# Kernel optimization log

Measured on AMD Instinct MI355X. Metric: run time of the kernel, lower is better.

The kernel has to match this reference:

```python
import jax, jax.numpy as jnp
import numpy as np

THR = 0.2          # config['thr']
BORDER_RM = 2      # config['border_rm']
TEMP = 0.1         # config['dsmax_temperature']


def setup_inputs() -> dict:
    key = jax.random.key(0)
    k0, k1 = jax.random.split(key)
    N, C = 2, 256
    h0c, w0c, h1c, w1c = 60, 80, 60, 80
    return {
        "feat_c0": jax.random.normal(k0, (N, h0c * w0c, C), dtype=jnp.float32),
        "feat_c1": jax.random.normal(k1, (N, h1c * w1c, C), dtype=jnp.float32),
        "h0c": h0c, "w0c": w0c, "h1c": h1c, "w1c": w1c,
    }


def _valid_1d(n: int, b: int):
    # True in the interior [b, n-b), False on the border — matches mask_border writes
    return jnp.zeros((n,), dtype=bool).at[b:n - b].set(True)


def reference(feat_c0, feat_c1, h0c, w0c, h1c, w1c):
    N, L, C = feat_c0.shape
    S = feat_c1.shape[1]
    scale = 1.0 / (C ** 0.5)
    f0 = feat_c0 * scale
    f1 = feat_c1 * scale

    # similarity + dual softmax  -> conf_matrix [N, L, S]
    sim = jnp.einsum('nlc,nsc->nls', f0, f1) / TEMP
    conf = jax.nn.softmax(sim, axis=1) * jax.nn.softmax(sim, axis=2)

    # threshold + border removal (mask_border, vectorized as an interior mask)
    mask = conf > THR
    b = BORDER_RM
    border = (_valid_1d(h0c, b)[:, None, None, None]
              & _valid_1d(w0c, b)[None, :, None, None]
              & _valid_1d(h1c, b)[None, None, :, None]
              & _valid_1d(w1c, b)[None, None, None, :])  # [h0c,w0c,h1c,w1c]
    mask = (mask.reshape(N, h0c, w0c, h1c, w1c) & border[None]).reshape(N, L, S)

    # mutual nearest neighbor
    mask = mask \
        & (conf == conf.max(axis=2, keepdims=True)) \
        & (conf == conf.max(axis=1, keepdims=True))

    # match extraction, expressed densely (static shapes for jit):
    # mask_v[b,i] = row i of pair b has a match; j_ids its column; mconf its confidence
    mask_v = mask.any(axis=2)                               # [N, L]
    j_ids = jnp.argmax(mask, axis=2)                        # [N, L] (first True)
    mconf = jnp.take_along_axis(conf, j_ids[:, :, None], axis=2)[..., 0]
    mconf = jnp.where(mask_v, mconf, 0.0)                   # [N, L]

    # coarse keypoint coords for matched columns: (x, y) = (j % w1c, j // w1c)
    mkpts1_c = jnp.stack([j_ids % w1c, j_ids // w1c], axis=-1)  # [N, L, 2]

    return conf, mask_v, j_ids, mkpts1_c, mconf
```

## Files before the change

### kernel.cpp

```cpp
#include <hip/hip_runtime.h>

typedef _Float16 half8 __attribute__((ext_vector_type(8)));
typedef float f32x4 __attribute__((ext_vector_type(4)));

#define NB 2
#define LS 4800
#define CCH 256
#define W0 80
#define W1 80
#define THRV 0.2f
#define SQS 0.19764235376052370f

#define TN 38
#define PADL 4864
#define NWG (TN * TN * NB)
#define CPX (NWG / 8)

#define OF_RST  0
#define OF_CST  19200
#define OF_RWM  38400
#define OF_CAND 48000
#define OF_CLM  57600
#define OF_PROW 67200
#define OF_PCOL (67200 + 739328)
#define OF_AH   (67200 + 2*739328)
#define OF_BH   (OF_AH + 1228800)

#define O_MASKV 46080000ull
#define O_JIDS  46089600ull
#define O_MKPT  46099200ull
#define O_MCONF 46118400ull

__device__ __forceinline__ void load_lds16(const void* g, void* l) {
    __builtin_amdgcn_global_load_lds((const __attribute__((address_space(1))) void*)g,
                                     (__attribute__((address_space(3))) void*)l, 16, 0, 0);
}

__device__ __forceinline__ void swizzle_ids(int& n, int& by, int& bx) {
    const int orig = ((int)blockIdx.z * TN + (int)blockIdx.y) * TN + (int)blockIdx.x;
    const int wg = (orig & 7) * CPX + (orig >> 3);
    n = wg / (TN * TN);
    const int rem = wg % (TN * TN);
    by = rem / TN; bx = rem % TN;
}

__global__ __launch_bounds__(256) void conv_half(const float* __restrict__ A,
                                                 const float* __restrict__ B,
                                                 float* __restrict__ ws) {
    const int which = blockIdx.y;
    const float* src = which ? B : A;
    _Float16* dst = (_Float16*)(ws + (which ? OF_BH : OF_AH));
    const int idx = blockIdx.x * 256 + threadIdx.x;
    const float4 v = ((const float4*)src)[idx];
    union { _Float16 h[4]; uint2 u; } p;
    p.h[0] = (_Float16)(v.x * SQS);
    p.h[1] = (_Float16)(v.y * SQS);
    p.h[2] = (_Float16)(v.z * SQS);
    p.h[3] = (_Float16)(v.w * SQS);
    ((uint2*)dst)[idx] = p.u;
}

__device__ __forceinline__ void gemm_core(const _Float16* __restrict__ Ah,
                                          const _Float16* __restrict__ Bh,
                                          _Float16* smA, _Float16* smB,
                                          const int bx, const int by,
                                          const int tid, f32x4 (&acc)[4][4]) {
    const int lane = tid & 63, w = tid >> 6;
    const int wx = w & 1, wy = w >> 1;
    const int m = lane & 15, quad = lane >> 4;
    const int rr = lane >> 2;
    const int q = (lane & 3) ^ ((lane >> 3) & 3);

    const _Float16* ga[2];
    const _Float16* gb[2];
#pragma unroll
    for (int i = 0; i < 2; i++) {
        const int c = w * 2 + i;
        int gra = by * 128 + c * 16 + rr; gra = gra < LS ? gra : LS - 1;
        int grb = bx * 128 + c * 16 + rr; grb = grb < LS ? grb : LS - 1;
        ga[i] = Ah + (size_t)gra * CCH + q * 8;
        gb[i] = Bh + (size_t)grb * CCH + q * 8;
    }

#pragma unroll
    for (int i = 0; i < 2; i++) {
        const int c = w * 2 + i;
        load_lds16(ga[i], &smA[c * 512]);
        load_lds16(gb[i], &smB[c * 512]);
    }

    for (int kt = 0; kt < 8; kt++) {
        __syncthreads();
        const int cur = (kt & 1) * 4096;
        if (kt < 7) {
            const int nxt = 4096 - cur;
            const int ko = (kt + 1) * 32;
#pragma unroll
            for (int i = 0; i < 2; i++) {
                const int c = w * 2 + i;
                load_lds16(ga[i] + ko, &smA[nxt + c * 512]);
                load_lds16(gb[i] + ko, &smB[nxt + c * 512]);
            }
        }
        half8 Af[4], Bf[4];
#pragma unroll
        for (int a = 0; a < 4; a++) {
            const int rl = wy * 64 + a * 16 + m;
            const int sl = rl * 4 + (quad ^ ((rl >> 1) & 3));
            Af[a] = *(const half8*)&smA[cur + sl * 8];
        }
#pragma unroll
        for (int b = 0; b < 4; b++) {
            const int cl = wx * 64 + b * 16 + m;
            const int sl = cl * 4 + (quad ^ ((cl >> 1) & 3));
            Bf[b] = *(const half8*)&smB[cur + sl * 8];
        }
#pragma unroll
        for (int a = 0; a < 4; a++)
#pragma unroll
            for (int b = 0; b < 4; b++)
                acc[a][b] = __builtin_amdgcn_mfma_f32_16x16x32_f16(Af[a], Bf[b], acc[a][b], 0, 0, 0);
    }
    __syncthreads();
}

__global__ __launch_bounds__(256, 3) void gemm_stats(float* __restrict__ ws) {
    __shared__ __align__(16) union {
        struct { _Float16 A[8192]; _Float16 B[8192]; } st;
        struct { float rs[128][2][2]; float cs[128][2][2]; } red;
    } sm;
    int n, by, bx;
    swizzle_ids(n, by, bx);
    const _Float16* Ah = (const _Float16*)(ws + OF_AH) + (size_t)n * LS * CCH;
    const _Float16* Bh = (const _Float16*)(ws + OF_BH) + (size_t)n * LS * CCH;
    const int tid = threadIdx.x;
    const int lane = tid & 63, w = tid >> 6;
    const int wx = w & 1, wy = w >> 1;
    const int m = lane & 15, quad = lane >> 4;

    f32x4 acc[4][4];
    {
        f32x4 z = {0.f, 0.f, 0.f, 0.f};
#pragma unroll
        for (int a = 0; a < 4; a++)
#pragma unroll
            for (int b = 0; b < 4; b++) acc[a][b] = z;
    }
    gemm_core(Ah, Bh, sm.st.A, sm.st.B, bx, by, tid, acc);

    const int l0 = by * 128, s0 = bx * 128;
    bool bval[4];
#pragma unroll
    for (int b = 0; b < 4; b++) bval[b] = (s0 + wx * 64 + b * 16 + m) < LS;

    float T = -1e30f;
#pragma unroll
    for (int a = 0; a < 4; a++)
#pragma unroll
        for (int reg = 0; reg < 4; reg++) {
            if ((l0 + wy * 64 + a * 16 + quad * 4 + reg) < LS) {
#pragma unroll
                for (int b = 0; b < 4; b++)
                    if (bval[b]) T = fmaxf(T, acc[a][b][reg]);
            }
        }
#pragma unroll
    for (int d = 1; d < 64; d <<= 1) T = fmaxf(T, __shfl_xor(T, d, 64));

#pragma unroll
    for (int a = 0; a < 4; a++)
#pragma unroll
        for (int reg = 0; reg < 4; reg++) {
            const bool rv = (l0 + wy * 64 + a * 16 + quad * 4 + reg) < LS;
#pragma unroll
            for (int b = 0; b < 4; b++)
                acc[a][b][reg] = (rv && bval[b]) ? __expf(acc[a][b][reg] - T) : 0.f;
        }

#pragma unroll
    for (int a = 0; a < 4; a++)
#pragma unroll
        for (int reg = 0; reg < 4; reg++) {
            float s = acc[a][0][reg] + acc[a][1][reg] + acc[a][2][reg] + acc[a][3][reg];
#pragma unroll
            for (int d = 1; d < 16; d <<= 1) s += __shfl_xor(s, d, 64);
            if (m == 0) {
                const int rl = wy * 64 + a * 16 + quad * 4 + reg;
                sm.red.rs[rl][wx][0] = T; sm.red.rs[rl][wx][1] = s;
            }
        }
#pragma unroll
    for (int b = 0; b < 4; b++) {
        float s = 0.f;
#pragma unroll
        for (int a = 0; a < 4; a++)
#pragma unroll
            for (int reg = 0; reg < 4; reg++) s += acc[a][b][reg];
        s += __shfl_xor(s, 16, 64);
        s += __shfl_xor(s, 32, 64);
        if (quad == 0) {
            const int cl = wx * 64 + b * 16 + m;
            sm.red.cs[cl][wy][0] = T; sm.red.cs[cl][wy][1] = s;
        }
    }
    __syncthreads();
    if (tid < 128) {
        const float m0 = sm.red.rs[tid][0][0], v0 = sm.red.rs[tid][0][1];
        const float m1 = sm.red.rs[tid][1][0], v1 = sm.red.rs[tid][1][1];
        const float nm = fmaxf(m0, m1);
        const float s = v0 * __expf(m0 - nm) + v1 * __expf(m1 - nm);
        ((float2*)(ws + OF_PROW))[((size_t)n * PADL + by * 128 + tid) * TN + bx] = make_float2(nm, s);
    } else {
        const int t = tid - 128;
        const float m0 = sm.red.cs[t][0][0], v0 = sm.red.cs[t][0][1];
        const float m1 = sm.red.cs[t][1][0], v1 = sm.red.cs[t][1][1];
        const float nm = fmaxf(m0, m1);
        const float s = v0 * __expf(m0 - nm) + v1 * __expf(m1 - nm);
        ((float2*)(ws + OF_PCOL))[((size_t)n * PADL + bx * 128 + t) * TN + by] = make_float2(nm, s);
    }
}

__global__ __launch_bounds__(256) void combine_stats(float* __restrict__ ws) {
    const int idx = blockIdx.x * 256 + threadIdx.x;
    const int half_ = idx >= 9600;
    const int i = idx - half_ * 9600;
    const int n = i / LS, r = i % LS;
    const float2* P = (const float2*)(ws + (half_ ? OF_PCOL : OF_PROW)) + ((size_t)n * PADL + r) * TN;
    float M = -1e30f, S = 0.f;
    for (int b = 0; b < TN; b++) {
        const float2 p = P[b];
        const float nm = fmaxf(M, p.x);
        S = S * __expf(M - nm) + p.y * __expf(p.x - nm);
        M = nm;
    }
    ((float2*)(ws + (half_ ? OF_CST : OF_RST)))[n * LS + r] = make_float2(M, 1.0f / S);
}

__global__ __launch_bounds__(256, 3) void gemm_conf(float* __restrict__ out,
                                                    float* __restrict__ ws) {
    __shared__ __align__(16) union {
        struct { _Float16 A[8192]; _Float16 B[8192]; } st;
        struct { float rst[128][2]; float cst[128][2];
                 float rsv[128][2][2]; float csv[128][2]; } ep;
    } sm;
    int n, by, bx;
    swizzle_ids(n, by, bx);
    const _Float16* Ah = (const _Float16*)(ws + OF_AH) + (size_t)n * LS * CCH;
    const _Float16* Bh = (const _Float16*)(ws + OF_BH) + (size_t)n * LS * CCH;
    const int tid = threadIdx.x;
    const int lane = tid & 63, w = tid >> 6;
    const int wx = w & 1, wy = w >> 1;
    const int m = lane & 15, quad = lane >> 4;

    f32x4 acc[4][4];
    {
        f32x4 z = {0.f, 0.f, 0.f, 0.f};
#pragma unroll
        for (int a = 0; a < 4; a++)
#pragma unroll
            for (int b = 0; b < 4; b++) acc[a][b] = z;
    }
    gemm_core(Ah, Bh, sm.st.A, sm.st.B, bx, by, tid, acc);

    const int l0 = by * 128, s0 = bx * 128;
    if (tid < 128) {
        int r = l0 + tid; r = r < LS ? r : LS - 1;
        const float2 v = ((const float2*)(ws + OF_RST))[n * LS + r];
        sm.ep.rst[tid][0] = v.x; sm.ep.rst[tid][1] = v.y;
    } else {
        const int t = tid - 128;
        int c = s0 + t; c = c < LS ? c : LS - 1;
        const float2 v = ((const float2*)(ws + OF_CST))[n * LS + c];
        sm.ep.cst[t][0] = v.x; sm.ep.cst[t][1] = v.y;
    }
    __syncthreads();

    float* On = out + (size_t)n * LS * LS;
    float colm[4] = {-1.f, -1.f, -1.f, -1.f};
    bool bval[4]; int gc4[4]; float cmx[4], csi[4];
#pragma unroll
    for (int b = 0; b < 4; b++) {
        const int cl = wx * 64 + b * 16 + m;
        gc4[b] = s0 + cl;
        bval[b] = gc4[b] < LS;
        cmx[b] = sm.ep.cst[cl][0]; csi[b] = sm.ep.cst[cl][1];
    }
#pragma unroll
    for (int a = 0; a < 4; a++) {
#pragma unroll
        for (int reg = 0; reg < 4; reg++) {
            const int rl = wy * 64 + a * 16 + quad * 4 + reg;
            const int gr = l0 + rl;
            const float rm = sm.ep.rst[rl][0], rsi = sm.ep.rst[rl][1];
            const bool rv = gr < LS;
            float bestv = -1.f; int besti = 0;
#pragma unroll
            for (int b = 0; b < 4; b++) {
                const float c = __expf(2.f * acc[a][b][reg] - rm - cmx[b]) * (rsi * csi[b]);
                if (rv && bval[b]) {
                    On[(size_t)gr * LS + gc4[b]] = c;
                    if (c > bestv) { bestv = c; besti = gc4[b]; }
                    colm[b] = fmaxf(colm[b], c);
                }
            }
#pragma unroll
            for (int d = 1; d < 16; d <<= 1) {
                const float ov = __shfl_xor(bestv, d, 64);
                const int oi = __shfl_xor(besti, d, 64);
                if (ov > bestv || (ov == bestv && oi < besti)) { bestv = ov; besti = oi; }
            }
            if (m == 0) {
                sm.ep.rsv[rl][wx][0] = bestv;
                sm.ep.rsv[rl][wx][1] = __int_as_float(besti);
            }
        }
    }
#pragma unroll
    for (int b = 0; b < 4; b++) {
        float v = colm[b];
        v = fmaxf(v, __shfl_xor(v, 16, 64));
        v = fmaxf(v, __shfl_xor(v, 32, 64));
        if (quad == 0) sm.ep.csv[wx * 64 + b * 16 + m][wy] = v;
    }
    __syncthreads();
    if (tid < 128) {
        const float v0 = sm.ep.rsv[tid][0][0]; const int i0 = __float_as_int(sm.ep.rsv[tid][0][1]);
        const float v1 = sm.ep.rsv[tid][1][0]; const int i1 = __float_as_int(sm.ep.rsv[tid][1][1]);
        float bv; int bi;
        if (v0 > v1 || (v0 == v1 && i0 <= i1)) { bv = v0; bi = i0; } else { bv = v1; bi = i1; }
        ((float2*)(ws + OF_PROW))[((size_t)n * PADL + by * 128 + tid) * TN + bx] =
            make_float2(bv, __int_as_float(bi));
    } else {
        const int t = tid - 128;
        const float v = fmaxf(sm.ep.csv[t][0], sm.ep.csv[t][1]);
        (ws + OF_PCOL)[((size_t)n * PADL + bx * 128 + t) * TN + by] = v;
    }
}

__global__ __launch_bounds__(256) void combine_max(float* __restrict__ ws) {
    const int idx = blockIdx.x * 256 + threadIdx.x;
    const int half_ = idx >= 9600;
    const int i = idx - half_ * 9600;
    const int n = i / LS, r = i % LS;
    if (!half_) {
        const float2* P = (const float2*)(ws + OF_PROW) + ((size_t)n * PADL + r) * TN;
        float bv = -2.f; int bi = 0;
        for (int b = 0; b < TN; b++) {
            const float2 p = P[b];
            const int pi = __float_as_int(p.y);
            if (p.x > bv || (p.x == bv && pi < bi)) { bv = p.x; bi = pi; }
        }
        ws[OF_RWM + i] = bv;
        ((int*)ws)[OF_CAND + i] = bi;
    } else {
        const float* P = ws + OF_PCOL + ((size_t)n * PADL + r) * TN;
        float v = -2.f;
        for (int b = 0; b < TN; b++) v = fmaxf(v, P[b]);
        ws[OF_CLM + i] = v;
    }
}

__global__ __launch_bounds__(256) void match_pass(const float* __restrict__ ws,
                                                  float* __restrict__ out) {
    const int idx = blockIdx.x * 256 + threadIdx.x;
    if (idx >= NB * LS) return;
    const int n = idx / LS, l = idx % LS;
    const float rwm = ws[OF_RWM + idx];
    const int cand = ((const int*)ws)[OF_CAND + idx];
    const float clm = ws[OF_CLM + n * LS + cand];
    const int y0 = l / W0, x0 = l % W0;
    const int y1 = cand / W1, x1 = cand % W1;
    const bool b0 = (y0 >= 2 && y0 < 58 && x0 >= 2 && x0 < 78);
    const bool b1 = (y1 >= 2 && y1 < 58 && x1 >= 2 && x1 < 78);
    const bool matched = (rwm > THRV) && b0 && b1 && (rwm == clm);
    const int j = matched ? cand : 0;
    out[O_MASKV + idx] = matched ? 1.f : 0.f;
    out[O_JIDS + idx] = (float)j;
    out[O_MKPT + (size_t)idx * 2 + 0] = (float)(j % W1);
    out[O_MKPT + (size_t)idx * 2 + 1] = (float)(j / W1);
    out[O_MCONF + idx] = matched ? rwm : 0.f;
}

extern "C" void kernel_launch(void* const* d_in, const int* in_sizes, int n_in,
                              void* d_out, int out_size, void* d_ws, size_t ws_size,
                              hipStream_t stream) {
    const float* f0 = (const float*)d_in[0];
    const float* f1 = (const float*)d_in[1];
    float* out = (float*)d_out;
    float* ws = (float*)d_ws;

    conv_half<<<dim3(2400, 2), 256, 0, stream>>>(f0, f1, ws);
    gemm_stats<<<dim3(TN, TN, NB), 256, 0, stream>>>(ws);
    combine_stats<<<75, 256, 0, stream>>>(ws);
    gemm_conf<<<dim3(TN, TN, NB), 256, 0, stream>>>(out, ws);
    combine_max<<<75, 256, 0, stream>>>(ws);
    match_pass<<<38, 256, 0, stream>>>(ws, out);
}
```

Measured before the change: 306.4 us.

## Use 256x128 GEMM tiles with 512-thread blocks and nontemporal conf stores

Doubles the row extent of each workgroup tile to 256 rows using 8 waves, so each B tile loaded into LDS is reused across twice as many rows. This halves the workgroup count and the number of column-statistics partials, and the partial reductions and the XCD swizzle are rewritten to match. The conf matrix output is now written with nontemporal stores to reduce cache pollution. Larger blocks and more LDS per block may lower occupancy, and the uneven XCD split adds some risk.

```diff
diff --git a/kernel.cpp b/kernel.cpp
--- a/kernel.cpp
+++ b/kernel.cpp
@@ -11,10 +11,10 @@
 #define THRV 0.2f
 #define SQS 0.19764235376052370f
 
-#define TN 38
+#define TN  38
+#define TNM 19
 #define PADL 4864
-#define NWG (TN * TN * NB)
-#define CPX (NWG / 8)
+#define NWG (TN * TNM * NB)
 
 #define OF_RST  0
 #define OF_CST  19200
@@ -37,10 +37,11 @@
 }
 
 __device__ __forceinline__ void swizzle_ids(int& n, int& by, int& bx) {
-    const int orig = ((int)blockIdx.z * TN + (int)blockIdx.y) * TN + (int)blockIdx.x;
-    const int wg = (orig & 7) * CPX + (orig >> 3);
-    n = wg / (TN * TN);
-    const int rem = wg % (TN * TN);
+    const int orig = ((int)blockIdx.z * TNM + (int)blockIdx.y) * TN + (int)blockIdx.x;
+    const int xcd = orig & 7, t = orig >> 3;
+    const int wg = (xcd < 4 ? xcd * 181 : 724 + (xcd - 4) * 180) + t;
+    n = wg / (TN * TNM);
+    const int rem = wg % (TN * TNM);
     by = rem / TN; bx = rem % TN;
 }
 
@@ -72,48 +73,44 @@
     const int q = (lane & 3) ^ ((lane >> 3) & 3);
 
     const _Float16* ga[2];
-    const _Float16* gb[2];
-#pragma unroll
-    for (int i = 0; i < 2; i++) {
-        const int c = w * 2 + i;
-        int gra = by * 128 + c * 16 + rr; gra = gra < LS ? gra : LS - 1;
-        int grb = bx * 128 + c * 16 + rr; grb = grb < LS ? grb : LS - 1;
-        ga[i] = Ah + (size_t)gra * CCH + q * 8;
-        gb[i] = Bh + (size_t)grb * CCH + q * 8;
-    }
-
-#pragma unroll
-    for (int i = 0; i < 2; i++) {
-        const int c = w * 2 + i;
-        load_lds16(ga[i], &smA[c * 512]);
-        load_lds16(gb[i], &smB[c * 512]);
-    }
+    const _Float16* gb0;
+    {
+#pragma unroll
+        for (int i = 0; i < 2; i++) {
+            const int c = w * 2 + i;
+            int gra = by * 256 + c * 16 + rr; gra = gra < LS ? gra : LS - 1;
+            ga[i] = Ah + (size_t)gra * CCH + q * 8;
+        }
+        int grb = bx * 128 + w * 16 + rr; grb = grb < LS ? grb : LS - 1;
+        gb0 = Bh + (size_t)grb * CCH + q * 8;
+    }
+
+#pragma unroll
+    for (int i = 0; i < 2; i++) load_lds16(ga[i], &smA[(w * 2 + i) * 512]);
+    load_lds16(gb0, &smB[w * 512]);
 
     for (int kt = 0; kt < 8; kt++) {
         __syncthreads();
-        const int cur = (kt & 1) * 4096;
+        const int curA = (kt & 1) * 8192, curB = (kt & 1) * 4096;
         if (kt < 7) {
-            const int nxt = 4096 - cur;
             const int ko = (kt + 1) * 32;
 #pragma unroll
-            for (int i = 0; i < 2; i++) {
-                const int c = w * 2 + i;
-                load_lds16(ga[i] + ko, &smA[nxt + c * 512]);
-                load_lds16(gb[i] + ko, &smB[nxt + c * 512]);
-            }
+            for (int i = 0; i < 2; i++)
+                load_lds16(ga[i] + ko, &smA[(8192 - curA) + (w * 2 + i) * 512]);
+            load_lds16(gb0 + ko, &smB[(4096 - curB) + w * 512]);
         }
         half8 Af[4], Bf[4];
 #pragma unroll
         for (int a = 0; a < 4; a++) {
             const int rl = wy * 64 + a * 16 + m;
             const int sl = rl * 4 + (quad ^ ((rl >> 1) & 3));
-            Af[a] = *(const half8*)&smA[cur + sl * 8];
+            Af[a] = *(const half8*)&smA[curA + sl * 8];
         }
 #pragma unroll
         for (int b = 0; b < 4; b++) {
             const int cl = wx * 64 + b * 16 + m;
             const int sl = cl * 4 + (quad ^ ((cl >> 1) & 3));
-            Bf[b] = *(const half8*)&smB[cur + sl * 8];
+            Bf[b] = *(const half8*)&smB[curB + sl * 8];
         }
 #pragma unroll
         for (int a = 0; a < 4; a++)
@@ -124,10 +121,10 @@
     __syncthreads();
 }
 
-__global__ __launch_bounds__(256, 3) void gemm_stats(float* __restrict__ ws) {
+__global__ __launch_bounds__(512, 4) void gemm_stats(float* __restrict__ ws) {
     __shared__ __align__(16) union {
-        struct { _Float16 A[8192]; _Float16 B[8192]; } st;
-        struct { float rs[128][2][2]; float cs[128][2][2]; } red;
+        struct { _Float16 A[2][8192]; _Float16 B[2][4096]; } st;
+        struct { float rs[256][2][2]; float cs[128][4][2]; } red;
     } sm;
     int n, by, bx;
     swizzle_ids(n, by, bx);
@@ -146,9 +143,9 @@
 #pragma unroll
             for (int b = 0; b < 4; b++) acc[a][b] = z;
     }
-    gemm_core(Ah, Bh, sm.st.A, sm.st.B, bx, by, tid, acc);
-
-    const int l0 = by * 128, s0 = bx * 128;
+    gemm_core(Ah, Bh, &sm.st.A[0][0], &sm.st.B[0][0], bx, by, tid, acc);
+
+    const int l0 = by * 256, s0 = bx * 128;
     bool bval[4];
 #pragma unroll
     for (int b = 0; b < 4; b++) bval[b] = (s0 + wx * 64 + b * 16 + m) < LS;
@@ -204,19 +201,23 @@
         }
     }
     __syncthreads();
-    if (tid < 128) {
+    if (tid < 256) {
         const float m0 = sm.red.rs[tid][0][0], v0 = sm.red.rs[tid][0][1];
         const float m1 = sm.red.rs[tid][1][0], v1 = sm.red.rs[tid][1][1];
         const float nm = fmaxf(m0, m1);
         const float s = v0 * __expf(m0 - nm) + v1 * __expf(m1 - nm);
-        ((float2*)(ws + OF_PROW))[((size_t)n * PADL + by * 128 + tid) * TN + bx] = make_float2(nm, s);
-    } else {
-        const int t = tid - 128;
-        const float m0 = sm.red.cs[t][0][0], v0 = sm.red.cs[t][0][1];
-        const float m1 = sm.red.cs[t][1][0], v1 = sm.red.cs[t][1][1];
-        const float nm = fmaxf(m0, m1);
-        const float s = v0 * __expf(m0 - nm) + v1 * __expf(m1 - nm);
-        ((float2*)(ws + OF_PCOL))[((size_t)n * PADL + bx * 128 + t) * TN + by] = make_float2(nm, s);
+        ((float2*)(ws + OF_PROW))[((size_t)n * PADL + l0 + tid) * TN + bx] = make_float2(nm, s);
+    } else if (tid < 384) {
+        const int t = tid - 256;
+        float M = sm.red.cs[t][0][0], S = sm.red.cs[t][0][1];
+#pragma unroll
+        for (int k = 1; k < 4; k++) {
+            const float mo = sm.red.cs[t][k][0], so = sm.red.cs[t][k][1];
+            const float nm = fmaxf(M, mo);
+            S = S * __expf(M - nm) + so * __expf(mo - nm);
+            M = nm;
+        }
+        ((float2*)(ws + OF_PCOL))[((size_t)n * PADL + s0 + t) * TNM + by] = make_float2(M, S);
     }
 }
 
@@ -225,23 +226,34 @@
     const int half_ = idx >= 9600;
     const int i = idx - half_ * 9600;
     const int n = i / LS, r = i % LS;
-    const float2* P = (const float2*)(ws + (half_ ? OF_PCOL : OF_PROW)) + ((size_t)n * PADL + r) * TN;
     float M = -1e30f, S = 0.f;
-    for (int b = 0; b < TN; b++) {
-        const float2 p = P[b];
-        const float nm = fmaxf(M, p.x);
-        S = S * __expf(M - nm) + p.y * __expf(p.x - nm);
-        M = nm;
-    }
-    ((float2*)(ws + (half_ ? OF_CST : OF_RST)))[n * LS + r] = make_float2(M, 1.0f / S);
-}
-
-__global__ __launch_bounds__(256, 3) void gemm_conf(float* __restrict__ out,
+    if (!half_) {
+        const float2* P = (const float2*)(ws + OF_PROW) + ((size_t)n * PADL + r) * TN;
+        for (int b = 0; b < TN; b++) {
+            const float2 p = P[b];
+            const float nm = fmaxf(M, p.x);
+            S = S * __expf(M - nm) + p.y * __expf(p.x - nm);
+            M = nm;
+        }
+        ((float2*)(ws + OF_RST))[n * LS + r] = make_float2(M, 1.0f / S);
+    } else {
+        const float2* P = (const float2*)(ws + OF_PCOL) + ((size_t)n * PADL + r) * TNM;
+        for (int b = 0; b < TNM; b++) {
+            const float2 p = P[b];
+            const float nm = fmaxf(M, p.x);
+            S = S * __expf(M - nm) + p.y * __expf(p.x - nm);
+            M = nm;
+        }
+        ((float2*)(ws + OF_CST))[n * LS + r] = make_float2(M, 1.0f / S);
+    }
+}
+
+__global__ __launch_bounds__(512, 4) void gemm_conf(float* __restrict__ out,
                                                     float* __restrict__ ws) {
     __shared__ __align__(16) union {
-        struct { _Float16 A[8192]; _Float16 B[8192]; } st;
-        struct { float rst[128][2]; float cst[128][2];
-                 float rsv[128][2][2]; float csv[128][2]; } ep;
+        struct { _Float16 A[2][8192]; _Float16 B[2][4096]; } st;
+        struct { float rst[256][2]; float cst[128][2];
+                 float rsv[256][2][2]; float csv[128][4]; } ep;
     } sm;
     int n, by, bx;
     swizzle_ids(n, by, bx);
@@ -260,15 +272,15 @@
 #pragma unroll
             for (int b = 0; b < 4; b++) acc[a][b] = z;
     }
-    gemm_core(Ah, Bh, sm.st.A, sm.st.B, bx, by, tid, acc);
-
-    const int l0 = by * 128, s0 = bx * 128;
-    if (tid < 128) {
+    gemm_core(Ah, Bh, &sm.st.A[0][0], &sm.st.B[0][0], bx, by, tid, acc);
+
+    const int l0 = by * 256, s0 = bx * 128;
+    if (tid < 256) {
         int r = l0 + tid; r = r < LS ? r : LS - 1;
         const float2 v = ((const float2*)(ws + OF_RST))[n * LS + r];
         sm.ep.rst[tid][0] = v.x; sm.ep.rst[tid][1] = v.y;
-    } else {
-        const int t = tid - 128;
+    } else if (tid < 384) {
+        const int t = tid - 256;
         int c = s0 + t; c = c < LS ? c : LS - 1;
         const float2 v = ((const float2*)(ws + OF_CST))[n * LS + c];
         sm.ep.cst[t][0] = v.x; sm.ep.cst[t][1] = v.y;
@@ -298,7 +310,7 @@
             for (int b = 0; b < 4; b++) {
                 const float c = __expf(2.f * acc[a][b][reg] - rm - cmx[b]) * (rsi * csi[b]);
                 if (rv && bval[b]) {
-                    On[(size_t)gr * LS + gc4[b]] = c;
+                    __builtin_nontemporal_store(c, &On[(size_t)gr * LS + gc4[b]]);
                     if (c > bestv) { bestv = c; besti = gc4[b]; }
                     colm[b] = fmaxf(colm[b], c);
                 }
@@ -323,17 +335,18 @@
         if (quad == 0) sm.ep.csv[wx * 64 + b * 16 + m][wy] = v;
     }
     __syncthreads();
-    if (tid < 128) {
+    if (tid < 256) {
         const float v0 = sm.ep.rsv[tid][0][0]; const int i0 = __float_as_int(sm.ep.rsv[tid][0][1]);
         const float v1 = sm.ep.rsv[tid][1][0]; const int i1 = __float_as_int(sm.ep.rsv[tid][1][1]);
         float bv; int bi;
         if (v0 > v1 || (v0 == v1 && i0 <= i1)) { bv = v0; bi = i0; } else { bv = v1; bi = i1; }
-        ((float2*)(ws + OF_PROW))[((size_t)n * PADL + by * 128 + tid) * TN + bx] =
+        ((float2*)(ws + OF_PROW))[((size_t)n * PADL + l0 + tid) * TN + bx] =
             make_float2(bv, __int_as_float(bi));
-    } else {
-        const int t = tid - 128;
-        const float v = fmaxf(sm.ep.csv[t][0], sm.ep.csv[t][1]);
-        (ws + OF_PCOL)[((size_t)n * PADL + bx * 128 + t) * TN + by] = v;
+    } else if (tid < 384) {
+        const int t = tid - 256;
+        const float v = fmaxf(fmaxf(sm.ep.csv[t][0], sm.ep.csv[t][1]),
+                              fmaxf(sm.ep.csv[t][2], sm.ep.csv[t][3]));
+        (ws + OF_PCOL)[((size_t)n * PADL + s0 + t) * TNM + by] = v;
     }
 }
 
@@ -353,9 +366,9 @@
         ws[OF_RWM + i] = bv;
         ((int*)ws)[OF_CAND + i] = bi;
     } else {
-        const float* P = ws + OF_PCOL + ((size_t)n * PADL + r) * TN;
+        const float* P = ws + OF_PCOL + ((size_t)n * PADL + r) * TNM;
         float v = -2.f;
-        for (int b = 0; b < TN; b++) v = fmaxf(v, P[b]);
+        for (int b = 0; b < TNM; b++) v = fmaxf(v, P[b]);
         ws[OF_CLM + i] = v;
     }
 }
@@ -390,9 +403,9 @@
     float* ws = (float*)d_ws;
 
     conv_half<<<dim3(2400, 2), 256, 0, stream>>>(f0, f1, ws);
-    gemm_stats<<<dim3(TN, TN, NB), 256, 0, stream>>>(ws);
+    gemm_stats<<<dim3(TN, TNM, NB), 512, 0, stream>>>(ws);
     combine_stats<<<75, 256, 0, stream>>>(ws);
-    gemm_conf<<<dim3(TN, TN, NB), 256, 0, stream>>>(out, ws);
+    gemm_conf<<<dim3(TN, TNM, NB), 512, 0, stream>>>(out, ws);
     combine_max<<<75, 256, 0, stream>>>(ws);
     match_pass<<<38, 256, 0, stream>>>(ws, out);
 }
```

New measurement: 310.6 us. About the same (+1.4%).

## Use 8 waves per GEMM tile and add mask-free fast path for interior tiles

Applied to the files above, without the earlier changes.

Both GEMM kernels go from 256 to 512 threads per 128x128 tile. Each wave now covers 32x64 instead of 64x64, so accumulator registers per thread halve and more waves can hide latency. The cross-wave column reductions are widened from 2 to 4 partials to match. Interior tiles skip the per-element bounds checks in the softmax-statistics and confidence epilogues. The cost is less MFMA work per wave between barriers, with more synchronisation and LDS traffic relative to compute.

```diff
diff --git a/kernel.cpp b/kernel.cpp
--- a/kernel.cpp
+++ b/kernel.cpp
@@ -64,48 +64,34 @@
                                           const _Float16* __restrict__ Bh,
                                           _Float16* smA, _Float16* smB,
                                           const int bx, const int by,
-                                          const int tid, f32x4 (&acc)[4][4]) {
+                                          const int tid, f32x4 (&acc)[2][4]) {
     const int lane = tid & 63, w = tid >> 6;
     const int wx = w & 1, wy = w >> 1;
     const int m = lane & 15, quad = lane >> 4;
     const int rr = lane >> 2;
     const int q = (lane & 3) ^ ((lane >> 3) & 3);
 
-    const _Float16* ga[2];
-    const _Float16* gb[2];
-#pragma unroll
-    for (int i = 0; i < 2; i++) {
-        const int c = w * 2 + i;
-        int gra = by * 128 + c * 16 + rr; gra = gra < LS ? gra : LS - 1;
-        int grb = bx * 128 + c * 16 + rr; grb = grb < LS ? grb : LS - 1;
-        ga[i] = Ah + (size_t)gra * CCH + q * 8;
-        gb[i] = Bh + (size_t)grb * CCH + q * 8;
-    }
-
-#pragma unroll
-    for (int i = 0; i < 2; i++) {
-        const int c = w * 2 + i;
-        load_lds16(ga[i], &smA[c * 512]);
-        load_lds16(gb[i], &smB[c * 512]);
-    }
+    int gra = by * 128 + w * 16 + rr; gra = gra < LS ? gra : LS - 1;
+    int grb = bx * 128 + w * 16 + rr; grb = grb < LS ? grb : LS - 1;
+    const _Float16* ga = Ah + (size_t)gra * CCH + q * 8;
+    const _Float16* gb = Bh + (size_t)grb * CCH + q * 8;
+
+    load_lds16(ga, &smA[w * 512]);
+    load_lds16(gb, &smB[w * 512]);
 
     for (int kt = 0; kt < 8; kt++) {
         __syncthreads();
         const int cur = (kt & 1) * 4096;
         if (kt < 7) {
+            const int ko = (kt + 1) * 32;
             const int nxt = 4096 - cur;
-            const int ko = (kt + 1) * 32;
-#pragma unroll
-            for (int i = 0; i < 2; i++) {
-                const int c = w * 2 + i;
-                load_lds16(ga[i] + ko, &smA[nxt + c * 512]);
-                load_lds16(gb[i] + ko, &smB[nxt + c * 512]);
-            }
-        }
-        half8 Af[4], Bf[4];
-#pragma unroll
-        for (int a = 0; a < 4; a++) {
-            const int rl = wy * 64 + a * 16 + m;
+            load_lds16(ga + ko, &smA[nxt + w * 512]);
+            load_lds16(gb + ko, &smB[nxt + w * 512]);
+        }
+        half8 Af[2], Bf[4];
+#pragma unroll
+        for (int a = 0; a < 2; a++) {
+            const int rl = wy * 32 + a * 16 + m;
             const int sl = rl * 4 + (quad ^ ((rl >> 1) & 3));
             Af[a] = *(const half8*)&smA[cur + sl * 8];
         }
@@ -116,7 +102,7 @@
             Bf[b] = *(const half8*)&smB[cur + sl * 8];
         }
 #pragma unroll
-        for (int a = 0; a < 4; a++)
+        for (int a = 0; a < 2; a++)
 #pragma unroll
             for (int b = 0; b < 4; b++)
                 acc[a][b] = __builtin_amdgcn_mfma_f32_16x16x32_f16(Af[a], Bf[b], acc[a][b], 0, 0, 0);
@@ -124,10 +110,10 @@
     __syncthreads();
 }
 
-__global__ __launch_bounds__(256, 3) void gemm_stats(float* __restrict__ ws) {
+__global__ __launch_bounds__(512, 6) void gemm_stats(float* __restrict__ ws) {
     __shared__ __align__(16) union {
-        struct { _Float16 A[8192]; _Float16 B[8192]; } st;
-        struct { float rs[128][2][2]; float cs[128][2][2]; } red;
+        struct { _Float16 A[2][4096]; _Float16 B[2][4096]; } st;
+        struct { float rs[128][2][2]; float cs[128][4][2]; } red;
     } sm;
     int n, by, bx;
     swizzle_ids(n, by, bx);
@@ -138,54 +124,77 @@
     const int wx = w & 1, wy = w >> 1;
     const int m = lane & 15, quad = lane >> 4;
 
-    f32x4 acc[4][4];
+    f32x4 acc[2][4];
     {
         f32x4 z = {0.f, 0.f, 0.f, 0.f};
 #pragma unroll
-        for (int a = 0; a < 4; a++)
+        for (int a = 0; a < 2; a++)
 #pragma unroll
             for (int b = 0; b < 4; b++) acc[a][b] = z;
     }
-    gemm_core(Ah, Bh, sm.st.A, sm.st.B, bx, by, tid, acc);
+    gemm_core(Ah, Bh, &sm.st.A[0][0], &sm.st.B[0][0], bx, by, tid, acc);
 
     const int l0 = by * 128, s0 = bx * 128;
-    bool bval[4];
-#pragma unroll
-    for (int b = 0; b < 4; b++) bval[b] = (s0 + wx * 64 + b * 16 + m) < LS;
+    const bool full = (by < 37) & (bx < 37);
 
     float T = -1e30f;
-#pragma unroll
-    for (int a = 0; a < 4; a++)
-#pragma unroll
-        for (int reg = 0; reg < 4; reg++) {
-            if ((l0 + wy * 64 + a * 16 + quad * 4 + reg) < LS) {
+    if (full) {
+#pragma unroll
+        for (int a = 0; a < 2; a++)
+#pragma unroll
+            for (int reg = 0; reg < 4; reg++)
+#pragma unroll
+                for (int b = 0; b < 4; b++) T = fmaxf(T, acc[a][b][reg]);
+    } else {
+        bool bval[4];
+#pragma unroll
+        for (int b = 0; b < 4; b++) bval[b] = (s0 + wx * 64 + b * 16 + m) < LS;
+#pragma unroll
+        for (int a = 0; a < 2; a++)
+#pragma unroll
+            for (int reg = 0; reg < 4; reg++) {
+                if ((l0 + wy * 32 + a * 16 + quad * 4 + reg) < LS) {
+#pragma unroll
+                    for (int b = 0; b < 4; b++)
+                        if (bval[b]) T = fmaxf(T, acc[a][b][reg]);
+                }
+            }
+    }
+#pragma unroll
+    for (int d = 1; d < 64; d <<= 1) T = fmaxf(T, __shfl_xor(T, d, 64));
+
+    if (full) {
+#pragma unroll
+        for (int a = 0; a < 2; a++)
+#pragma unroll
+            for (int reg = 0; reg < 4; reg++)
 #pragma unroll
                 for (int b = 0; b < 4; b++)
-                    if (bval[b]) T = fmaxf(T, acc[a][b][reg]);
+                    acc[a][b][reg] = __expf(acc[a][b][reg] - T);
+    } else {
+        bool bval[4];
+#pragma unroll
+        for (int b = 0; b < 4; b++) bval[b] = (s0 + wx * 64 + b * 16 + m) < LS;
+#pragma unroll
+        for (int a = 0; a < 2; a++)
+#pragma unroll
+            for (int reg = 0; reg < 4; reg++) {
+                const bool rv = (l0 + wy * 32 + a * 16 + quad * 4 + reg) < LS;
+#pragma unroll
+                for (int b = 0; b < 4; b++)
+                    acc[a][b][reg] = (rv && bval[b]) ? __expf(acc[a][b][reg] - T) : 0.f;
             }
-        }
-#pragma unroll
-    for (int d = 1; d < 64; d <<= 1) T = fmaxf(T, __shfl_xor(T, d, 64));
-
-#pragma unroll
-    for (int a = 0; a < 4; a++)
-#pragma unroll
-        for (int reg = 0; reg < 4; reg++) {
-            const bool rv = (l0 + wy * 64 + a * 16 + quad * 4 + reg) < LS;
-#pragma unroll
-            for (int b = 0; b < 4; b++)
-                acc[a][b][reg] = (rv && bval[b]) ? __expf(acc[a][b][reg] - T) : 0.f;
-        }
-
-#pragma unroll
-    for (int a = 0; a < 4; a++)
+    }
+
+#pragma unroll
+    for (int a = 0; a < 2; a++)
 #pragma unroll
         for (int reg = 0; reg < 4; reg++) {
             float s = acc[a][0][reg] + acc[a][1][reg] + acc[a][2][reg] + acc[a][3][reg];
 #pragma unroll
             for (int d = 1; d < 16; d <<= 1) s += __shfl_xor(s, d, 64);
             if (m == 0) {
-                const int rl = wy * 64 + a * 16 + quad * 4 + reg;
+                const int rl = wy * 32 + a * 16 + quad * 4 + reg;
                 sm.red.rs[rl][wx][0] = T; sm.red.rs[rl][wx][1] = s;
             }
         }
@@ -193,7 +202,7 @@
     for (int b = 0; b < 4; b++) {
         float s = 0.f;
 #pragma unroll
-        for (int a = 0; a < 4; a++)
+        for (int a = 0; a < 2; a++)
 #pragma unroll
             for (int reg = 0; reg < 4; reg++) s += acc[a][b][reg];
         s += __shfl_xor(s, 16, 64);
@@ -209,14 +218,18 @@
         const float m1 = sm.red.rs[tid][1][0], v1 = sm.red.rs[tid][1][1];
         const float nm = fmaxf(m0, m1);
         const float s = v0 * __expf(m0 - nm) + v1 * __expf(m1 - nm);
-        ((float2*)(ws + OF_PROW))[((size_t)n * PADL + by * 128 + tid) * TN + bx] = make_float2(nm, s);
-    } else {
+        ((float2*)(ws + OF_PROW))[((size_t)n * PADL + l0 + tid) * TN + bx] = make_float2(nm, s);
+    } else if (tid < 256) {
         const int t = tid - 128;
-        const float m0 = sm.red.cs[t][0][0], v0 = sm.red.cs[t][0][1];
-        const float m1 = sm.red.cs[t][1][0], v1 = sm.red.cs[t][1][1];
-        const float nm = fmaxf(m0, m1);
-        const float s = v0 * __expf(m0 - nm) + v1 * __expf(m1 - nm);
-        ((float2*)(ws + OF_PCOL))[((size_t)n * PADL + bx * 128 + t) * TN + by] = make_float2(nm, s);
+        float M = sm.red.cs[t][0][0], S = sm.red.cs[t][0][1];
+#pragma unroll
+        for (int k = 1; k < 4; k++) {
+            const float mo = sm.red.cs[t][k][0], so = sm.red.cs[t][k][1];
+            const float nm = fmaxf(M, mo);
+            S = S * __expf(M - nm) + so * __expf(mo - nm);
+            M = nm;
+        }
+        ((float2*)(ws + OF_PCOL))[((size_t)n * PADL + s0 + t) * TN + by] = make_float2(M, S);
     }
 }
 
@@ -236,12 +249,12 @@
     ((float2*)(ws + (half_ ? OF_CST : OF_RST)))[n * LS + r] = make_float2(M, 1.0f / S);
 }
 
-__global__ __launch_bounds__(256, 3) void gemm_conf(float* __restrict__ out,
+__global__ __launch_bounds__(512, 6) void gemm_conf(float* __restrict__ out,
                                                     float* __restrict__ ws) {
     __shared__ __align__(16) union {
-        struct { _Float16 A[8192]; _Float16 B[8192]; } st;
+        struct { _Float16 A[2][4096]; _Float16 B[2][4096]; } st;
         struct { float rst[128][2]; float cst[128][2];
-                 float rsv[128][2][2]; float csv[128][2]; } ep;
+                 float rsv[128][2][2]; float csv[128][4]; } ep;
     } sm;
     int n, by, bx;
     swizzle_ids(n, by, bx);
@@ -252,22 +265,23 @@
     const int wx = w & 1, wy = w >> 1;
     const int m = lane & 15, quad = lane >> 4;
 
-    f32x4 acc[4][4];
+    f32x4 acc[2][4];
     {
         f32x4 z = {0.f, 0.f, 0.f, 0.f};
 #pragma unroll
-        for (int a = 0; a < 4; a++)
+        for (int a = 0; a < 2; a++)
 #pragma unroll
             for (int b = 0; b < 4; b++) acc[a][b] = z;
     }
-    gemm_core(Ah, Bh, sm.st.A, sm.st.B, bx, by, tid, acc);
+    gemm_core(Ah, Bh, &sm.st.A[0][0], &sm.st.B[0][0], bx, by, tid, acc);
 
     const int l0 = by * 128, s0 = bx * 128;
+    const bool full = (by < 37) & (bx < 37);
     if (tid < 128) {
         int r = l0 + tid; r = r < LS ? r : LS - 1;
         const float2 v = ((const float2*)(ws + OF_RST))[n * LS + r];
         sm.ep.rst[tid][0] = v.x; sm.ep.rst[tid][1] = v.y;
-    } else {
+    } else if (tid < 256) {
         const int t = tid - 128;
         int c = s0 + t; c = c < LS ? c : LS - 1;
         const float2 v = ((const float2*)(ws + OF_CST))[n * LS + c];
@@ -277,41 +291,73 @@
 
     float* On = out + (size_t)n * LS * LS;
     float colm[4] = {-1.f, -1.f, -1.f, -1.f};
-    bool bval[4]; int gc4[4]; float cmx[4], csi[4];
+    int gc4[4]; float cmx[4], csi[4];
 #pragma unroll
     for (int b = 0; b < 4; b++) {
         const int cl = wx * 64 + b * 16 + m;
         gc4[b] = s0 + cl;
-        bval[b] = gc4[b] < LS;
         cmx[b] = sm.ep.cst[cl][0]; csi[b] = sm.ep.cst[cl][1];
     }
-#pragma unroll
-    for (int a = 0; a < 4; a++) {
-#pragma unroll
-        for (int reg = 0; reg < 4; reg++) {
-            const int rl = wy * 64 + a * 16 + quad * 4 + reg;
-            const int gr = l0 + rl;
-            const float rm = sm.ep.rst[rl][0], rsi = sm.ep.rst[rl][1];
-            const bool rv = gr < LS;
-            float bestv = -1.f; int besti = 0;
-#pragma unroll
-            for (int b = 0; b < 4; b++) {
-                const float c = __expf(2.f * acc[a][b][reg] - rm - cmx[b]) * (rsi * csi[b]);
-                if (rv && bval[b]) {
+    if (full) {
+#pragma unroll
+        for (int a = 0; a < 2; a++) {
+#pragma unroll
+            for (int reg = 0; reg < 4; reg++) {
+                const int rl = wy * 32 + a * 16 + quad * 4 + reg;
+                const int gr = l0 + rl;
+                const float rm = sm.ep.rst[rl][0], rsi = sm.ep.rst[rl][1];
+                float bestv = -1.f; int besti = 0;
+#pragma unroll
+                for (int b = 0; b < 4; b++) {
+                    const float c = __expf(2.f * acc[a][b][reg] - rm - cmx[b]) * (rsi * csi[b]);
                     On[(size_t)gr * LS + gc4[b]] = c;
                     if (c > bestv) { bestv = c; besti = gc4[b]; }
                     colm[b] = fmaxf(colm[b], c);
                 }
+#pragma unroll
+                for (int d = 1; d < 16; d <<= 1) {
+                    const float ov = __shfl_xor(bestv, d, 64);
+                    const int oi = __shfl_xor(besti, d, 64);
+                    if (ov > bestv || (ov == bestv && oi < besti)) { bestv = ov; besti = oi; }
+                }
+                if (m == 0) {
+                    sm.ep.rsv[rl][wx][0] = bestv;
+                    sm.ep.rsv[rl][wx][1] = __int_as_float(besti);
+                }
             }
-#pragma unroll
-            for (int d = 1; d < 16; d <<= 1) {
-                const float ov = __shfl_xor(bestv, d, 64);
-                const int oi = __shfl_xor(besti, d, 64);
-                if (ov > bestv || (ov == bestv && oi < besti)) { bestv = ov; besti = oi; }
-            }
-            if (m == 0) {
-                sm.ep.rsv[rl][wx][0] = bestv;
-                sm.ep.rsv[rl][wx][1] = __int_as_float(besti);
+        }
+    } else {
+        bool bval[4];
+#pragma unroll
+        for (int b = 0; b < 4; b++) bval[b] = gc4[b] < LS;
+#pragma unroll
+        for (int a = 0; a < 2; a++) {
+#pragma unroll
+            for (int reg = 0; reg < 4; reg++) {
+                const int rl = wy * 32 + a * 16 + quad * 4 + reg;
+                const int gr = l0 + rl;
+                const float rm = sm.ep.rst[rl][0], rsi = sm.ep.rst[rl][1];
+                const bool rv = gr < LS;
+                float bestv = -1.f; int besti = 0;
+#pragma unroll
+                for (int b = 0; b < 4; b++) {
+                    const float c = __expf(2.f * acc[a][b][reg] - rm - cmx[b]) * (rsi * csi[b]);
+                    if (rv && bval[b]) {
+                        On[(size_t)gr * LS + gc4[b]] = c;
+                        if (c > bestv) { bestv = c; besti = gc4[b]; }
+                        colm[b] = fmaxf(colm[b], c);
+                    }
+                }
+#pragma unroll
+                for (int d = 1; d < 16; d <<= 1) {
+                    const float ov = __shfl_xor(bestv, d, 64);
+                    const int oi = __shfl_xor(besti, d, 64);
+                    if (ov > bestv || (ov == bestv && oi < besti)) { bestv = ov; besti = oi; }
+                }
+                if (m == 0) {
+                    sm.ep.rsv[rl][wx][0] = bestv;
+                    sm.ep.rsv[rl][wx][1] = __int_as_float(besti);
+                }
             }
         }
     }
@@ -328,12 +374,13 @@
         const float v1 = sm.ep.rsv[tid][1][0]; const int i1 = __float_as_int(sm.ep.rsv[tid][1][1]);
         float bv; int bi;
         if (v0 > v1 || (v0 == v1 && i0 <= i1)) { bv = v0; bi = i0; } else { bv = v1; bi = i1; }
-        ((float2*)(ws + OF_PROW))[((size_t)n * PADL + by * 128 + tid) * TN + bx] =
+        ((float2*)(ws + OF_PROW))[((size_t)n * PADL + l0 + tid) * TN + bx] =
             make_float2(bv, __int_as_float(bi));
-    } else {
+    } else if (tid < 256) {
         const int t = tid - 128;
-        const float v = fmaxf(sm.ep.csv[t][0], sm.ep.csv[t][1]);
-        (ws + OF_PCOL)[((size_t)n * PADL + bx * 128 + t) * TN + by] = v;
+        const float v = fmaxf(fmaxf(sm.ep.csv[t][0], sm.ep.csv[t][1]),
+                              fmaxf(sm.ep.csv[t][2], sm.ep.csv[t][3]));
+        (ws + OF_PCOL)[((size_t)n * PADL + s0 + t) * TN + by] = v;
     }
 }
 
@@ -390,9 +437,9 @@
     float* ws = (float*)d_ws;
 
     conv_half<<<dim3(2400, 2), 256, 0, stream>>>(f0, f1, ws);
-    gemm_stats<<<dim3(TN, TN, NB), 256, 0, stream>>>(ws);
+    gemm_stats<<<dim3(TN, TN, NB), 512, 0, stream>>>(ws);
     combine_stats<<<75, 256, 0, stream>>>(ws);
-    gemm_conf<<<dim3(TN, TN, NB), 256, 0, stream>>>(out, ws);
+    gemm_conf<<<dim3(TN, TN, NB), 512, 0, stream>>>(out, ws);
     combine_max<<<75, 256, 0, stream>>>(ws);
     match_pass<<<38, 256, 0, stream>>>(ws, out);
 }
```

After: 301.7 us. Within noise of the previous version (-1.5%).
